# Optimization experiments

Measured on AMD Instinct MI355X. Metric: run time of the kernel, lower is better.

Reference implementation:

```python
import math
import jax, jax.numpy as jnp
import numpy as np

H = 16
D_MODEL = 1024
D_K = D_MODEL // H


def setup_inputs() -> dict:
    key = jax.random.key(0)
    ks = jax.random.split(key, 16)
    B, S = 2, 2048
    s = 1.0 / math.sqrt(D_MODEL)
    inp = {
        "q": jax.random.normal(ks[0], (B, S, D_MODEL), jnp.float32),
        "k": jax.random.normal(ks[1], (B, S, D_MODEL), jnp.float32),
        "v": jax.random.normal(ks[2], (B, S, D_MODEL), jnp.float32),
        "mask": jax.random.randint(ks[3], (B, S), 0, 2, jnp.int32),
        "Wq": jax.random.normal(ks[4], (D_MODEL, D_MODEL), jnp.float32) * s,
        "bq": jnp.zeros((D_MODEL,), jnp.float32),
        "Wk": jax.random.normal(ks[5], (D_MODEL, D_MODEL), jnp.float32) * s,
        "bk": jnp.zeros((D_MODEL,), jnp.float32),
        "Wv": jax.random.normal(ks[6], (D_MODEL, D_MODEL), jnp.float32) * s,
        "bv": jnp.zeros((D_MODEL,), jnp.float32),
        "Wp": jax.random.normal(ks[7], (D_MODEL, D_MODEL), jnp.float32) * s,
        "bp": jnp.zeros((D_MODEL,), jnp.float32),
        "gamma": jnp.ones((D_MODEL,), jnp.float32),
        "beta": jnp.zeros((D_MODEL,), jnp.float32),
    }
    return inp


def reference(q, k, v, mask, Wq, bq, Wk, bk, Wv, bv, Wp, bp, gamma, beta):
    B, S, _ = q.shape
    residual = q
    # projections -> [B, H, S, D_K]
    def split_heads(x):
        return x.reshape(B, S, H, D_K).transpose(0, 2, 1, 3)
    qh = split_heads(q @ Wq + bq)
    kh = split_heads(k @ Wk + bk)
    vh = split_heads(v @ Wv + bv)
    # scores [B, H, S, S]
    scores = jnp.einsum("bhqd,bhkd->bhqk", qh, kh) / math.sqrt(D_K)
    m = mask[:, None, None, :]  # [B,1,1,S_k]
    scores = jnp.where(m == 0, -1e9, scores)
    attn = jax.nn.softmax(scores, axis=-1)  # dropout is identity in eval
    out = jnp.einsum("bhqk,bhkd->bhqd", attn, vh)
    out = out.transpose(0, 2, 1, 3).reshape(B, S, D_MODEL)
    out = out @ Wp + bp
    x = residual + out
    # LayerNorm over last dim, eps=1e-5 (torch default)
    mu = jnp.mean(x, axis=-1, keepdims=True)
    var = jnp.mean((x - mu) ** 2, axis=-1, keepdims=True)
    out = (x - mu) * jax.lax.rsqrt(var + 1e-5) * gamma + beta
    return (out, attn)
```

## Files before the change

kernel.cpp:

```cpp
#include <hip/hip_runtime.h>
#include <hip/hip_bf16.h>

#define HN 16
#define DM 1024
#define DKH 64
#define BB 2
#define SS 2048
#define NT (BB*SS)
#define BK 32

using bf16   = __bf16;
using bf16x4 = __attribute__((ext_vector_type(4))) __bf16;
using bf16x8 = __attribute__((ext_vector_type(8))) __bf16;
using f32x4  = __attribute__((ext_vector_type(4))) float;

__device__ __forceinline__ void gload16(bf16* lds, const bf16* g) {
    __builtin_amdgcn_global_load_lds(
        (const __attribute__((address_space(1))) unsigned int*)g,
        (__attribute__((address_space(3))) unsigned int*)lds, 16, 0, 0);
}

__global__ __launch_bounds__(256) void convert_qkv(
    const float* __restrict__ q, const float* __restrict__ k,
    const float* __restrict__ v, bf16* __restrict__ dst)
{
    const int z = blockIdx.z;
    const float* src = (z == 0) ? q : (z == 1) ? k : v;
    bf16* d = dst + (size_t)z * NT * DM;
    int i = blockIdx.x * 256 + threadIdx.x;
    const int n4 = NT * DM / 4;
    if (i < n4) {
        float4 f = ((const float4*)src)[i];
        bf16x4 o = { (bf16)f.x, (bf16)f.y, (bf16)f.z, (bf16)f.w };
        ((bf16x4*)d)[i] = o;
    }
}

__global__ __launch_bounds__(256) void transpose_w(
    const float* __restrict__ Wq, const float* __restrict__ Wk,
    const float* __restrict__ Wv, const float* __restrict__ Wp,
    bf16* __restrict__ dst)
{
    const int z = blockIdx.z;
    const float* W = (z == 0) ? Wq : (z == 1) ? Wk : (z == 2) ? Wv : Wp;
    bf16* WT = dst + (size_t)z * DM * DM;
    __shared__ float t[64][65];
    const int tx = threadIdx.x;
    const int r0 = blockIdx.y * 64, c0 = blockIdx.x * 64;
    {
        const int row = tx >> 2, cb = (tx & 3) * 16;
        const float4* src = (const float4*)(W + (size_t)(r0 + row) * DM + c0 + cb);
        #pragma unroll
        for (int i = 0; i < 4; i++) {
            float4 f = src[i];
            t[row][cb + i*4 + 0] = f.x; t[row][cb + i*4 + 1] = f.y;
            t[row][cb + i*4 + 2] = f.z; t[row][cb + i*4 + 3] = f.w;
        }
    }
    __syncthreads();
    {
        const int n = tx >> 2, kb = (tx & 3) * 16;
        bf16 buf[16];
        #pragma unroll
        for (int i = 0; i < 16; i++) buf[i] = (bf16)t[kb + i][n];
        bf16* outp = WT + (size_t)(c0 + n) * DM + r0 + kb;
        *(bf16x8*)(outp)     = *(bf16x8*)(&buf[0]);
        *(bf16x8*)(outp + 8) = *(bf16x8*)(&buf[8]);
    }
}

__device__ __forceinline__ void gemm_core_128(
    const bf16* __restrict__ A, const bf16* __restrict__ Bt,
    int row0, int col0, bf16* As, bf16* Bs, f32x4 (&acc)[4][4])
{
    const int t = threadIdx.x;
    const int lane = t & 63, w = t >> 6;
    const int wr = w >> 1, wc = w & 1;
    const int lg = lane >> 4, l16 = lane & 15;
    const int srow = lane >> 2, scol = (lane & 3) * 8;
    const bf16* gA0 = A  + (size_t)(row0 + w*32 +      srow) * DM + scol;
    const bf16* gA1 = A  + (size_t)(row0 + w*32 + 16 + srow) * DM + scol;
    const bf16* gB0 = Bt + (size_t)(col0 + w*32 +      srow) * DM + scol;
    const bf16* gB1 = Bt + (size_t)(col0 + w*32 + 16 + srow) * DM + scol;
    bf16* lA0 = As + (w*32     ) * BK;
    bf16* lA1 = As + (w*32 + 16) * BK;
    bf16* lB0 = Bs + (w*32     ) * BK;
    bf16* lB1 = Bs + (w*32 + 16) * BK;

    for (int k0 = 0; k0 < DM; k0 += BK) {
        gload16(lA0, gA0 + k0);
        gload16(lA1, gA1 + k0);
        gload16(lB0, gB0 + k0);
        gload16(lB1, gB1 + k0);
        __syncthreads();
        bf16x8 af[4], bfr[4];
        #pragma unroll
        for (int m = 0; m < 4; m++)
            af[m] = *(const bf16x8*)(As + (wr*64 + m*16 + l16) * BK + lg*8);
        #pragma unroll
        for (int n = 0; n < 4; n++)
            bfr[n] = *(const bf16x8*)(Bs + (wc*64 + n*16 + l16) * BK + lg*8);
        #pragma unroll
        for (int m = 0; m < 4; m++)
            #pragma unroll
            for (int n = 0; n < 4; n++)
                acc[m][n] = __builtin_amdgcn_mfma_f32_16x16x32_bf16(af[m], bfr[n], acc[m][n], 0, 0, 0);
        __syncthreads();
    }
}

__global__ __launch_bounds__(256) void gemm_qkv(
    const bf16* __restrict__ qkvb, const bf16* __restrict__ wT,
    const float* __restrict__ bq, const float* __restrict__ bk,
    const float* __restrict__ bv, bf16* __restrict__ outbase)
{
    __shared__ __align__(16) bf16 As[128 * BK];
    __shared__ __align__(16) bf16 Bs[128 * BK];
    const int z = blockIdx.z;
    const bf16* A;
    const bf16* Bt;
    int row0, col0;
    if (z != 2) {
        A    = qkvb + (size_t)z * NT * DM;
        Bt   = wT   + (size_t)z * DM * DM;
        row0 = blockIdx.y * 128;
        col0 = blockIdx.x * 128;
    } else {
        A    = wT   + (size_t)2 * DM * DM;
        Bt   = qkvb + (size_t)2 * NT * DM;
        row0 = blockIdx.x * 128;
        col0 = blockIdx.y * 128;
    }

    f32x4 acc[4][4] = {};
    gemm_core_128(A, Bt, row0, col0, As, Bs, acc);

    const int t = threadIdx.x, lane = t & 63, w = t >> 6;
    const int wr = w >> 1, wc = w & 1, lg = lane >> 4, l16 = lane & 15;

    if (z == 0) {
        bf16* outp = outbase;
        const float qscale = 0.125f * 1.44269504f;
        #pragma unroll
        for (int m = 0; m < 4; m++) {
            #pragma unroll
            for (int n = 0; n < 4; n++) {
                const int col = col0 + wc*64 + n*16 + l16;
                const float bcol = bq[col];
                const int h = col >> 6, dk = col & 63;
                #pragma unroll
                for (int r = 0; r < 4; r++) {
                    const int row = row0 + wr*64 + m*16 + lg*4 + r;
                    const int b = row >> 11, s = row & (SS - 1);
                    const float val = (acc[m][n][r] + bcol) * qscale;
                    outp[(((size_t)b*HN + h)*SS + s)*DKH + dk] = (bf16)val;
                }
            }
        }
    } else if (z == 1) {
        bf16* outp = outbase + (size_t)NT * DM;
        #pragma unroll
        for (int m = 0; m < 4; m++) {
            #pragma unroll
            for (int n = 0; n < 4; n++) {
                const int col = col0 + wc*64 + n*16 + l16;
                const float bcol = bk[col];
                const int h = col >> 6, d = col & 63;
                #pragma unroll
                for (int r = 0; r < 4; r++) {
                    const int row = row0 + wr*64 + m*16 + lg*4 + r;
                    const int b = row >> 11, s = row & (SS - 1);
                    const float val = acc[m][n][r] + bcol;
                    const size_t bh = (size_t)b*HN + h;
                    const size_t idx = bh*SS*DKH
                        + (size_t)(((s>>4)*2 + (d>>5))*512)
                        + ((s&15)*4 + ((d>>3)&3))*8 + (d&7);
                    outp[idx] = (bf16)val;
                }
            }
        }
    } else {
        bf16* outp = outbase + (size_t)2 * NT * DM;
        #pragma unroll
        for (int m = 0; m < 4; m++) {
            #pragma unroll
            for (int n = 0; n < 4; n++) {
                const int tok = col0 + wc*64 + n*16 + l16;
                const int b = tok >> 11, s = tok & (SS - 1);
                #pragma unroll
                for (int r = 0; r < 4; r++) {
                    const int hdk = row0 + wr*64 + m*16 + lg*4 + r;
                    const int h = hdk >> 6, dk = hdk & 63;
                    const float val = acc[m][n][r] + bv[hdk];
                    const size_t bh = (size_t)b*HN + h;
                    const size_t idx = bh*SS*DKH
                        + (size_t)(((s>>5)*4 + (dk>>4))*512)
                        + ((dk&15)*4 + ((s>>3)&3))*8 + (s&7);
                    outp[idx] = (bf16)val;
                }
            }
        }
    }
}

__global__ __launch_bounds__(256) void attn_kernel(
    const bf16* __restrict__ Qh, const bf16* __restrict__ Kswz,
    const bf16* __restrict__ Vswz, const int* __restrict__ mask,
    float* __restrict__ attn, bf16* __restrict__ Ob)
{
    __shared__ float bias_s[SS];
    const int hwid = blockIdx.x;
    const int vid  = (hwid & 7) * 64 + (hwid >> 3);
    const int bh = vid >> 4;
    const int b  = bh >> 4;
    const int q0 = (vid & 15) * 128;
    const bf16* Kb = Kswz + (size_t)bh * SS * DKH;
    const bf16* Vb = Vswz + (size_t)bh * SS * DKH;
    const bf16* Q  = Qh   + (size_t)bh * SS * DKH;
    const int t = threadIdx.x, w = t >> 6, lane = t & 63;
    const int lg = lane >> 4, l16 = lane & 15;
    const int lp = (l16 << 2) | lg;

    for (int i = t; i < SS; i += 256)
        bias_s[i] = mask[b * SS + i] ? 0.0f : -1.44269504e9f;

    bf16x8 qf[2][2];
    #pragma unroll
    for (int tl = 0; tl < 2; tl++) {
        const bf16* qp = Q + (size_t)(q0 + w*32 + tl*16 + l16)*DKH + lg*8;
        qf[tl][0] = *(const bf16x8*)(qp);
        qf[tl][1] = *(const bf16x8*)(qp + 32);
    }
    __syncthreads();

    float l_[2] = {0.f, 0.f};
    bf16x8 kc0 = *(const bf16x8*)(Kb + lp*8);
    bf16x8 kc1 = *(const bf16x8*)(Kb + 512 + lp*8);
    for (int c = 0; c < 128; c++) {
        const int cn = (c + 1 < 128) ? c + 1 : 127;
        bf16x8 kn0 = *(const bf16x8*)(Kb + (size_t)(cn*2    )*512 + lp*8);
        bf16x8 kn1 = *(const bf16x8*)(Kb + (size_t)(cn*2 + 1)*512 + lp*8);
        const float4 b4 = *(const float4*)(&bias_s[c*16 + lg*4]);
        #pragma unroll
        for (int tl = 0; tl < 2; tl++) {
            f32x4 st = {0.f, 0.f, 0.f, 0.f};
            st = __builtin_amdgcn_mfma_f32_16x16x32_bf16(kc0, qf[tl][0], st, 0, 0, 0);
            st = __builtin_amdgcn_mfma_f32_16x16x32_bf16(kc1, qf[tl][1], st, 0, 0, 0);
            l_[tl] += exp2f(st[0] + b4.x) + exp2f(st[1] + b4.y)
                    + exp2f(st[2] + b4.z) + exp2f(st[3] + b4.w);
        }
        kc0 = kn0; kc1 = kn1;
    }
    float inv_l[2];
    #pragma unroll
    for (int tl = 0; tl < 2; tl++) {
        float l = l_[tl];
        l += __shfl_xor(l, 16);
        l += __shfl_xor(l, 32);
        inv_l[tl] = 1.0f / l;
    }

    float* attn_base = attn + ((size_t)bh * SS + q0 + w*32) * SS;
    f32x4 oacc[2][4] = {};
    const int srcA = ((((2*lg)    ) & 3)*16 + l16) << 2;
    const int srcB = ((((2*lg) + 1) & 3)*16 + l16) << 2;
    const bool selT = (lg >= 2);
    const int  kseg = lane & 7;
    const bool selS = (kseg >> 2) != 0;
    const int  srow8 = lane >> 3;
    const int srcS0 = ((kseg & 3)*16 +     srow8) << 2;
    const int srcS1 = ((kseg & 3)*16 + 8 + srow8) << 2;

    bf16x8 ck[4], cv[4];
    #pragma unroll
    for (int h = 0; h < 4; h++) ck[h] = *(const bf16x8*)(Kb + (size_t)h*512 + lp*8);
    #pragma unroll
    for (int n = 0; n < 4; n++) cv[n] = *(const bf16x8*)(Vb + (size_t)n*512 + lp*8);

    for (int j = 0; j < 64; j++) {
        bf16x8 nk[4], nv[4];
        const bool have = (j + 1) < 64;
        if (have) {
            #pragma unroll
            for (int h = 0; h < 4; h++)
                nk[h] = *(const bf16x8*)(Kb + (size_t)((j+1)*4 + h)*512 + lp*8);
            #pragma unroll
            for (int n = 0; n < 4; n++)
                nv[n] = *(const bf16x8*)(Vb + (size_t)((j+1)*4 + n)*512 + lp*8);
        }
        const float4 b40 = *(const float4*)(&bias_s[(2*j    )*16 + lg*4]);
        const float4 b41 = *(const float4*)(&bias_s[(2*j + 1)*16 + lg*4]);
        #pragma unroll
        for (int tl = 0; tl < 2; tl++) {
            f32x4 s0 = {0.f, 0.f, 0.f, 0.f};
            s0 = __builtin_amdgcn_mfma_f32_16x16x32_bf16(ck[0], qf[tl][0], s0, 0, 0, 0);
            s0 = __builtin_amdgcn_mfma_f32_16x16x32_bf16(ck[1], qf[tl][1], s0, 0, 0, 0);
            f32x4 s1 = {0.f, 0.f, 0.f, 0.f};
            s1 = __builtin_amdgcn_mfma_f32_16x16x32_bf16(ck[2], qf[tl][0], s1, 0, 0, 0);
            s1 = __builtin_amdgcn_mfma_f32_16x16x32_bf16(ck[3], qf[tl][1], s1, 0, 0, 0);
            const float p00 = exp2f(s0[0] + b40.x), p01 = exp2f(s0[1] + b40.y);
            const float p02 = exp2f(s0[2] + b40.z), p03 = exp2f(s0[3] + b40.w);
            const float p10 = exp2f(s1[0] + b41.x), p11 = exp2f(s1[1] + b41.y);
            const float p12 = exp2f(s1[2] + b41.z), p13 = exp2f(s1[3] + b41.w);
            bf16x4 pk0 = { (bf16)p00, (bf16)p01, (bf16)p02, (bf16)p03 };
            bf16x4 pk1 = { (bf16)p10, (bf16)p11, (bf16)p12, (bf16)p13 };
            int2 k0d = *(int2*)&pk0;
            int2 k1d = *(int2*)&pk1;
            int dd0t0 = __builtin_amdgcn_ds_bpermute(srcA, k0d.x);
            int dd0t1 = __builtin_amdgcn_ds_bpermute(srcA, k1d.x);
            int dd1t0 = __builtin_amdgcn_ds_bpermute(srcA, k0d.y);
            int dd1t1 = __builtin_amdgcn_ds_bpermute(srcA, k1d.y);
            int dd2t0 = __builtin_amdgcn_ds_bpermute(srcB, k0d.x);
            int dd2t1 = __builtin_amdgcn_ds_bpermute(srcB, k1d.x);
            int dd3t0 = __builtin_amdgcn_ds_bpermute(srcB, k0d.y);
            int dd3t1 = __builtin_amdgcn_ds_bpermute(srcB, k1d.y);
            union { int4 i; bf16x8 h; } pa;
            pa.i.x = selT ? dd0t1 : dd0t0;
            pa.i.y = selT ? dd1t1 : dd1t0;
            pa.i.z = selT ? dd2t1 : dd2t0;
            pa.i.w = selT ? dd3t1 : dd3t0;
            #pragma unroll
            for (int n = 0; n < 4; n++)
                oacc[tl][n] = __builtin_amdgcn_mfma_f32_16x16x32_bf16(pa.h, cv[n], oacc[tl][n], 0, 0, 0);
            const float il = inv_l[tl];
            f32x4 pv0 = { p00*il, p01*il, p02*il, p03*il };
            f32x4 pv1 = { p10*il, p11*il, p12*il, p13*il };
            #pragma unroll
            for (int i = 0; i < 2; i++) {
                const int srcS = i ? srcS1 : srcS0;
                f32x4 outv;
                #pragma unroll
                for (int d = 0; d < 4; d++) {
                    int v0 = __builtin_amdgcn_ds_bpermute(srcS, __float_as_int(pv0[d]));
                    int v1 = __builtin_amdgcn_ds_bpermute(srcS, __float_as_int(pv1[d]));
                    outv[d] = __int_as_float(selS ? v1 : v0);
                }
                *(f32x4*)(attn_base + (size_t)(tl*16 + i*8 + srow8)*SS + j*32 + kseg*4) = outv;
            }
        }
        #pragma unroll
        for (int h = 0; h < 4; h++) ck[h] = nk[h];
        #pragma unroll
        for (int n = 0; n < 4; n++) cv[n] = nv[n];
    }

    const int hh = bh & 15;
    #pragma unroll
    for (int tl = 0; tl < 2; tl++) {
        #pragma unroll
        for (int r = 0; r < 4; r++) {
            const float il = __shfl(inv_l[tl], lg*4 + r);
            const int srow = q0 + w*32 + tl*16 + lg*4 + r;
            #pragma unroll
            for (int n = 0; n < 4; n++) {
                const float val = oacc[tl][n][r] * il;
                Ob[((size_t)b*SS + srow)*DM + hh*DKH + n*16 + l16] = (bf16)val;
            }
        }
    }
}

__global__ __launch_bounds__(256) void gemm_out(
    const bf16* __restrict__ Ob, const bf16* __restrict__ WpT,
    const float* __restrict__ bp, const float* __restrict__ resid,
    float* __restrict__ out)
{
    __shared__ __align__(16) bf16 As[128 * BK];
    __shared__ __align__(16) bf16 Bs[128 * BK];
    const int row0 = blockIdx.y * 128, col0 = blockIdx.x * 128;
    f32x4 acc[4][4] = {};
    gemm_core_128(Ob, WpT, row0, col0, As, Bs, acc);

    const int t = threadIdx.x, lane = t & 63, w = t >> 6;
    const int wr = w >> 1, wc = w & 1, lg = lane >> 4, l16 = lane & 15;
    #pragma unroll
    for (int m = 0; m < 4; m++) {
        #pragma unroll
        for (int n = 0; n < 4; n++) {
            const int col = col0 + wc*64 + n*16 + l16;
            const float bcol = bp[col];
            #pragma unroll
            for (int r = 0; r < 4; r++) {
                const int row = row0 + wr*64 + m*16 + lg*4 + r;
                const size_t idx = (size_t)row * DM + col;
                out[idx] = acc[m][n][r] + bcol + resid[idx];
            }
        }
    }
}

__global__ __launch_bounds__(256) void ln_kernel(
    float* __restrict__ x, const float* __restrict__ gamma,
    const float* __restrict__ beta)
{
    const int row = blockIdx.x, t = threadIdx.x;
    float4 v = ((const float4*)(x + (size_t)row * DM))[t];
    float s  = v.x + v.y + v.z + v.w;
    float s2 = v.x*v.x + v.y*v.y + v.z*v.z + v.w*v.w;
    #pragma unroll
    for (int off = 32; off; off >>= 1) {
        s  += __shfl_xor(s, off);
        s2 += __shfl_xor(s2, off);
    }
    __shared__ float rs_[4], rs2_[4];
    const int w = t >> 6;
    if ((t & 63) == 0) { rs_[w] = s; rs2_[w] = s2; }
    __syncthreads();
    s  = rs_[0] + rs_[1] + rs_[2] + rs_[3];
    s2 = rs2_[0] + rs2_[1] + rs2_[2] + rs2_[3];
    const float mu   = s * (1.0f / DM);
    const float var  = s2 * (1.0f / DM) - mu * mu;
    const float rstd = rsqrtf(var + 1e-5f);
    float4 g  = ((const float4*)gamma)[t];
    float4 bb = ((const float4*)beta)[t];
    float4 o;
    o.x = (v.x - mu) * rstd * g.x + bb.x;
    o.y = (v.y - mu) * rstd * g.y + bb.y;
    o.z = (v.z - mu) * rstd * g.z + bb.z;
    o.w = (v.w - mu) * rstd * g.w + bb.w;
    ((float4*)(x + (size_t)row * DM))[t] = o;
}

extern "C" void kernel_launch(void* const* d_in, const int* in_sizes, int n_in,
                              void* d_out, int out_size, void* d_ws, size_t ws_size,
                              hipStream_t stream)
{
    const float* q     = (const float*)d_in[0];
    const float* k     = (const float*)d_in[1];
    const float* v     = (const float*)d_in[2];
    const int*   mask  = (const int*)  d_in[3];
    const float* Wq    = (const float*)d_in[4];
    const float* bq    = (const float*)d_in[5];
    const float* Wk    = (const float*)d_in[6];
    const float* bk    = (const float*)d_in[7];
    const float* Wv    = (const float*)d_in[8];
    const float* bv    = (const float*)d_in[9];
    const float* Wp    = (const float*)d_in[10];
    const float* bp    = (const float*)d_in[11];
    const float* gamma = (const float*)d_in[12];
    const float* beta  = (const float*)d_in[13];

    float* out  = (float*)d_out;
    float* attn = out + (size_t)NT * DM;

    char* wsb = (char*)d_ws;
    bf16* qb   = (bf16*)wsb;
    bf16* wT   = (bf16*)(wsb + 25165824);
    bf16* Qh   = (bf16*)(wsb + 33554432);
    bf16* Ob   = (bf16*)(wsb + 58720256);
    bf16* Kswz = Qh + (size_t)NT * DM;
    bf16* Vswz = Qh + (size_t)2 * NT * DM;

    convert_qkv<<<dim3(4096, 1, 3), 256, 0, stream>>>(q, k, v, qb);
    transpose_w<<<dim3(16, 16, 4), 256, 0, stream>>>(Wq, Wk, Wv, Wp, wT);
    gemm_qkv   <<<dim3(8, 32, 3),  256, 0, stream>>>(qb, wT, bq, bk, bv, Qh);
    attn_kernel<<<dim3(512, 1),    256, 0, stream>>>(Qh, Kswz, Vswz, mask, attn, Ob);
    gemm_out   <<<dim3(8, 32),     256, 0, stream>>>(Ob, wT + 3*1048576, bp, q, out);
    ln_kernel  <<<4096,            256, 0, stream>>>(out, gamma, beta);
}
```

Before: 325.0 us.

## Halve attention query tile per block to double grid size and occupancy

Each attention block now handles 64 query rows (16 per wave) instead of 128, so the grid grows from 512 to 1024 blocks and the per-wave two-tile loop collapses to a single tile. The launch bounds gain a min-blocks hint of 4 to cap register use and raise occupancy. The aim is to fill the 256 CUs more evenly and hide the memory latency of the large attn-matrix writes. In exchange, each K/V tile is reused by half as many queries, so K/V global reads roughly double and the mask-bias LDS setup is repeated per block.

Result: slower. 384.5 us (+18.3%).

```diff
diff --git a/kernel.cpp b/kernel.cpp
--- a/kernel.cpp
+++ b/kernel.cpp
@@ -203,17 +203,17 @@
     }
 }
 
-__global__ __launch_bounds__(256) void attn_kernel(
+__global__ __launch_bounds__(256, 4) void attn_kernel(
     const bf16* __restrict__ Qh, const bf16* __restrict__ Kswz,
     const bf16* __restrict__ Vswz, const int* __restrict__ mask,
     float* __restrict__ attn, bf16* __restrict__ Ob)
 {
     __shared__ float bias_s[SS];
     const int hwid = blockIdx.x;
-    const int vid  = (hwid & 7) * 64 + (hwid >> 3);
-    const int bh = vid >> 4;
+    const int vid  = (hwid & 7) * 128 + (hwid >> 3);
+    const int bh = vid >> 5;
     const int b  = bh >> 4;
-    const int q0 = (vid & 15) * 128;
+    const int q0 = (vid & 31) * 64;
     const bf16* Kb = Kswz + (size_t)bh * SS * DKH;
     const bf16* Vb = Vswz + (size_t)bh * SS * DKH;
     const bf16* Q  = Qh   + (size_t)bh * SS * DKH;
@@ -224,16 +224,15 @@
     for (int i = t; i < SS; i += 256)
         bias_s[i] = mask[b * SS + i] ? 0.0f : -1.44269504e9f;
 
-    bf16x8 qf[2][2];
-    #pragma unroll
-    for (int tl = 0; tl < 2; tl++) {
-        const bf16* qp = Q + (size_t)(q0 + w*32 + tl*16 + l16)*DKH + lg*8;
-        qf[tl][0] = *(const bf16x8*)(qp);
-        qf[tl][1] = *(const bf16x8*)(qp + 32);
+    bf16x8 qf[2];
+    {
+        const bf16* qp = Q + (size_t)(q0 + w*16 + l16)*DKH + lg*8;
+        qf[0] = *(const bf16x8*)(qp);
+        qf[1] = *(const bf16x8*)(qp + 32);
     }
     __syncthreads();
 
-    float l_[2] = {0.f, 0.f};
+    float l_ = 0.f;
     bf16x8 kc0 = *(const bf16x8*)(Kb + lp*8);
     bf16x8 kc1 = *(const bf16x8*)(Kb + 512 + lp*8);
     for (int c = 0; c < 128; c++) {
@@ -241,27 +240,23 @@
         bf16x8 kn0 = *(const bf16x8*)(Kb + (size_t)(cn*2    )*512 + lp*8);
         bf16x8 kn1 = *(const bf16x8*)(Kb + (size_t)(cn*2 + 1)*512 + lp*8);
         const float4 b4 = *(const float4*)(&bias_s[c*16 + lg*4]);
-        #pragma unroll
-        for (int tl = 0; tl < 2; tl++) {
-            f32x4 st = {0.f, 0.f, 0.f, 0.f};
-            st = __builtin_amdgcn_mfma_f32_16x16x32_bf16(kc0, qf[tl][0], st, 0, 0, 0);
-            st = __builtin_amdgcn_mfma_f32_16x16x32_bf16(kc1, qf[tl][1], st, 0, 0, 0);
-            l_[tl] += exp2f(st[0] + b4.x) + exp2f(st[1] + b4.y)
-                    + exp2f(st[2] + b4.z) + exp2f(st[3] + b4.w);
-        }
+        f32x4 st = {0.f, 0.f, 0.f, 0.f};
+        st = __builtin_amdgcn_mfma_f32_16x16x32_bf16(kc0, qf[0], st, 0, 0, 0);
+        st = __builtin_amdgcn_mfma_f32_16x16x32_bf16(kc1, qf[1], st, 0, 0, 0);
+        l_ += exp2f(st[0] + b4.x) + exp2f(st[1] + b4.y)
+            + exp2f(st[2] + b4.z) + exp2f(st[3] + b4.w);
         kc0 = kn0; kc1 = kn1;
     }
-    float inv_l[2];
-    #pragma unroll
-    for (int tl = 0; tl < 2; tl++) {
-        float l = l_[tl];
+    float inv_l;
+    {
+        float l = l_;
         l += __shfl_xor(l, 16);
         l += __shfl_xor(l, 32);
-        inv_l[tl] = 1.0f / l;
-    }
-
-    float* attn_base = attn + ((size_t)bh * SS + q0 + w*32) * SS;
-    f32x4 oacc[2][4] = {};
+        inv_l = 1.0f / l;
+    }
+
+    float* attn_base = attn + ((size_t)bh * SS + q0 + w*16) * SS;
+    f32x4 oacc[4] = {};
     const int srcA = ((((2*lg)    ) & 3)*16 + l16) << 2;
     const int srcB = ((((2*lg) + 1) & 3)*16 + l16) << 2;
     const bool selT = (lg >= 2);
@@ -290,14 +285,13 @@
         }
         const float4 b40 = *(const float4*)(&bias_s[(2*j    )*16 + lg*4]);
         const float4 b41 = *(const float4*)(&bias_s[(2*j + 1)*16 + lg*4]);
-        #pragma unroll
-        for (int tl = 0; tl < 2; tl++) {
+        {
             f32x4 s0 = {0.f, 0.f, 0.f, 0.f};
-            s0 = __builtin_amdgcn_mfma_f32_16x16x32_bf16(ck[0], qf[tl][0], s0, 0, 0, 0);
-            s0 = __builtin_amdgcn_mfma_f32_16x16x32_bf16(ck[1], qf[tl][1], s0, 0, 0, 0);
+            s0 = __builtin_amdgcn_mfma_f32_16x16x32_bf16(ck[0], qf[0], s0, 0, 0, 0);
+            s0 = __builtin_amdgcn_mfma_f32_16x16x32_bf16(ck[1], qf[1], s0, 0, 0, 0);
             f32x4 s1 = {0.f, 0.f, 0.f, 0.f};
-            s1 = __builtin_amdgcn_mfma_f32_16x16x32_bf16(ck[2], qf[tl][0], s1, 0, 0, 0);
-            s1 = __builtin_amdgcn_mfma_f32_16x16x32_bf16(ck[3], qf[tl][1], s1, 0, 0, 0);
+            s1 = __builtin_amdgcn_mfma_f32_16x16x32_bf16(ck[2], qf[0], s1, 0, 0, 0);
+            s1 = __builtin_amdgcn_mfma_f32_16x16x32_bf16(ck[3], qf[1], s1, 0, 0, 0);
             const float p00 = exp2f(s0[0] + b40.x), p01 = exp2f(s0[1] + b40.y);
             const float p02 = exp2f(s0[2] + b40.z), p03 = exp2f(s0[3] + b40.w);
             const float p10 = exp2f(s1[0] + b41.x), p11 = exp2f(s1[1] + b41.y);
@@ -321,8 +315,8 @@
             pa.i.w = selT ? dd3t1 : dd3t0;
             #pragma unroll
             for (int n = 0; n < 4; n++)
-                oacc[tl][n] = __builtin_amdgcn_mfma_f32_16x16x32_bf16(pa.h, cv[n], oacc[tl][n], 0, 0, 0);
-            const float il = inv_l[tl];
+                oacc[n] = __builtin_amdgcn_mfma_f32_16x16x32_bf16(pa.h, cv[n], oacc[n], 0, 0, 0);
+            const float il = inv_l;
             f32x4 pv0 = { p00*il, p01*il, p02*il, p03*il };
             f32x4 pv1 = { p10*il, p11*il, p12*il, p13*il };
             #pragma unroll
@@ -335,7 +329,7 @@
                     int v1 = __builtin_amdgcn_ds_bpermute(srcS, __float_as_int(pv1[d]));
                     outv[d] = __int_as_float(selS ? v1 : v0);
                 }
-                *(f32x4*)(attn_base + (size_t)(tl*16 + i*8 + srow8)*SS + j*32 + kseg*4) = outv;
+                *(f32x4*)(attn_base + (size_t)(i*8 + srow8)*SS + j*32 + kseg*4) = outv;
             }
         }
         #pragma unroll
@@ -346,16 +340,13 @@
 
     const int hh = bh & 15;
     #pragma unroll
-    for (int tl = 0; tl < 2; tl++) {
-        #pragma unroll
-        for (int r = 0; r < 4; r++) {
-            const float il = __shfl(inv_l[tl], lg*4 + r);
-            const int srow = q0 + w*32 + tl*16 + lg*4 + r;
-            #pragma unroll
-            for (int n = 0; n < 4; n++) {
-                const float val = oacc[tl][n][r] * il;
-                Ob[((size_t)b*SS + srow)*DM + hh*DKH + n*16 + l16] = (bf16)val;
-            }
+    for (int r = 0; r < 4; r++) {
+        const float il = __shfl(inv_l, lg*4 + r);
+        const int srow = q0 + w*16 + lg*4 + r;
+        #pragma unroll
+        for (int n = 0; n < 4; n++) {
+            const float val = oacc[n][r] * il;
+            Ob[((size_t)b*SS + srow)*DM + hh*DKH + n*16 + l16] = (bf16)val;
         }
     }
 }
@@ -454,7 +445,7 @@
     convert_qkv<<<dim3(4096, 1, 3), 256, 0, stream>>>(q, k, v, qb);
     transpose_w<<<dim3(16, 16, 4), 256, 0, stream>>>(Wq, Wk, Wv, Wp, wT);
     gemm_qkv   <<<dim3(8, 32, 3),  256, 0, stream>>>(qb, wT, bq, bk, bv, Qh);
-    attn_kernel<<<dim3(512, 1),    256, 0, stream>>>(Qh, Kswz, Vswz, mask, attn, Ob);
+    attn_kernel<<<dim3(1024, 1),   256, 0, stream>>>(Qh, Kswz, Vswz, mask, attn, Ob);
     gemm_out   <<<dim3(8, 32),     256, 0, stream>>>(Ob, wT + 3*1048576, bp, q, out);
     ln_kernel  <<<4096,            256, 0, stream>>>(out, gamma, beta);
 }
```

## Split attention key range across two wave groups with LDS reduction

Applied to the files above, without the earlier changes.

The attention kernel now runs 512 threads per block: two groups of four waves each take half of the key sequence for both the row-sum pass and the P·V/attn-write pass. Partial row sums and partial output accumulators are combined through shared memory, with a sync between stages. The register double-buffered K/V prefetch is replaced by direct loads each iteration. The aim is more waves in flight per block, to hide memory latency on the large attn store. The cost is extra LDS, sync overhead, and register pressure under launch_bounds(512,4).

New measurement: 348.9 us. 1.07x slower.

```diff
diff --git a/kernel.cpp b/kernel.cpp
--- a/kernel.cpp
+++ b/kernel.cpp
@@ -203,12 +203,14 @@
     }
 }
 
-__global__ __launch_bounds__(256) void attn_kernel(
+__global__ __launch_bounds__(512, 4) void attn_kernel(
     const bf16* __restrict__ Qh, const bf16* __restrict__ Kswz,
     const bf16* __restrict__ Vswz, const int* __restrict__ mask,
     float* __restrict__ attn, bf16* __restrict__ Ob)
 {
     __shared__ float bias_s[SS];
+    __shared__ float l_red[2][4][2][16];
+    __shared__ float ored[4][32][68];
     const int hwid = blockIdx.x;
     const int vid  = (hwid & 7) * 64 + (hwid >> 3);
     const int bh = vid >> 4;
@@ -218,26 +220,28 @@
     const bf16* Vb = Vswz + (size_t)bh * SS * DKH;
     const bf16* Q  = Qh   + (size_t)bh * SS * DKH;
     const int t = threadIdx.x, w = t >> 6, lane = t & 63;
+    const int qw = w & 3, kw = w >> 2;
     const int lg = lane >> 4, l16 = lane & 15;
     const int lp = (l16 << 2) | lg;
 
-    for (int i = t; i < SS; i += 256)
+    for (int i = t; i < SS; i += 512)
         bias_s[i] = mask[b * SS + i] ? 0.0f : -1.44269504e9f;
 
     bf16x8 qf[2][2];
     #pragma unroll
     for (int tl = 0; tl < 2; tl++) {
-        const bf16* qp = Q + (size_t)(q0 + w*32 + tl*16 + l16)*DKH + lg*8;
+        const bf16* qp = Q + (size_t)(q0 + qw*32 + tl*16 + l16)*DKH + lg*8;
         qf[tl][0] = *(const bf16x8*)(qp);
         qf[tl][1] = *(const bf16x8*)(qp + 32);
     }
     __syncthreads();
 
+    const int c0 = kw * 64, c1 = c0 + 64;
     float l_[2] = {0.f, 0.f};
-    bf16x8 kc0 = *(const bf16x8*)(Kb + lp*8);
-    bf16x8 kc1 = *(const bf16x8*)(Kb + 512 + lp*8);
-    for (int c = 0; c < 128; c++) {
-        const int cn = (c + 1 < 128) ? c + 1 : 127;
+    bf16x8 kc0 = *(const bf16x8*)(Kb + (size_t)(c0*2    )*512 + lp*8);
+    bf16x8 kc1 = *(const bf16x8*)(Kb + (size_t)(c0*2 + 1)*512 + lp*8);
+    for (int c = c0; c < c1; c++) {
+        const int cn = (c + 1 < c1) ? c + 1 : c1 - 1;
         bf16x8 kn0 = *(const bf16x8*)(Kb + (size_t)(cn*2    )*512 + lp*8);
         bf16x8 kn1 = *(const bf16x8*)(Kb + (size_t)(cn*2 + 1)*512 + lp*8);
         const float4 b4 = *(const float4*)(&bias_s[c*16 + lg*4]);
@@ -251,16 +255,22 @@
         }
         kc0 = kn0; kc1 = kn1;
     }
+    #pragma unroll
+    for (int tl = 0; tl < 2; tl++) {
+        l_[tl] += __shfl_xor(l_[tl], 16);
+        l_[tl] += __shfl_xor(l_[tl], 32);
+    }
+    if (lane < 16) {
+        l_red[kw][qw][0][l16] = l_[0];
+        l_red[kw][qw][1][l16] = l_[1];
+    }
+    __syncthreads();
     float inv_l[2];
     #pragma unroll
-    for (int tl = 0; tl < 2; tl++) {
-        float l = l_[tl];
-        l += __shfl_xor(l, 16);
-        l += __shfl_xor(l, 32);
-        inv_l[tl] = 1.0f / l;
-    }
-
-    float* attn_base = attn + ((size_t)bh * SS + q0 + w*32) * SS;
+    for (int tl = 0; tl < 2; tl++)
+        inv_l[tl] = 1.0f / (l_[tl] + l_red[kw ^ 1][qw][tl][l16]);
+
+    float* attn_base = attn + ((size_t)bh * SS + q0 + qw*32) * SS;
     f32x4 oacc[2][4] = {};
     const int srcA = ((((2*lg)    ) & 3)*16 + l16) << 2;
     const int srcB = ((((2*lg) + 1) & 3)*16 + l16) << 2;
@@ -271,23 +281,15 @@
     const int srcS0 = ((kseg & 3)*16 +     srow8) << 2;
     const int srcS1 = ((kseg & 3)*16 + 8 + srow8) << 2;
 
-    bf16x8 ck[4], cv[4];
-    #pragma unroll
-    for (int h = 0; h < 4; h++) ck[h] = *(const bf16x8*)(Kb + (size_t)h*512 + lp*8);
-    #pragma unroll
-    for (int n = 0; n < 4; n++) cv[n] = *(const bf16x8*)(Vb + (size_t)n*512 + lp*8);
-
-    for (int j = 0; j < 64; j++) {
-        bf16x8 nk[4], nv[4];
-        const bool have = (j + 1) < 64;
-        if (have) {
-            #pragma unroll
-            for (int h = 0; h < 4; h++)
-                nk[h] = *(const bf16x8*)(Kb + (size_t)((j+1)*4 + h)*512 + lp*8);
-            #pragma unroll
-            for (int n = 0; n < 4; n++)
-                nv[n] = *(const bf16x8*)(Vb + (size_t)((j+1)*4 + n)*512 + lp*8);
-        }
+    const int j0 = kw * 32, j1 = j0 + 32;
+    for (int j = j0; j < j1; j++) {
+        bf16x8 ck[4], cv[4];
+        #pragma unroll
+        for (int h = 0; h < 4; h++)
+            ck[h] = *(const bf16x8*)(Kb + (size_t)(j*4 + h)*512 + lp*8);
+        #pragma unroll
+        for (int n = 0; n < 4; n++)
+            cv[n] = *(const bf16x8*)(Vb + (size_t)(j*4 + n)*512 + lp*8);
         const float4 b40 = *(const float4*)(&bias_s[(2*j    )*16 + lg*4]);
         const float4 b41 = *(const float4*)(&bias_s[(2*j + 1)*16 + lg*4]);
         #pragma unroll
@@ -338,23 +340,32 @@
                 *(f32x4*)(attn_base + (size_t)(tl*16 + i*8 + srow8)*SS + j*32 + kseg*4) = outv;
             }
         }
-        #pragma unroll
-        for (int h = 0; h < 4; h++) ck[h] = nk[h];
-        #pragma unroll
-        for (int n = 0; n < 4; n++) cv[n] = nv[n];
-    }
-
-    const int hh = bh & 15;
-    #pragma unroll
-    for (int tl = 0; tl < 2; tl++) {
-        #pragma unroll
-        for (int r = 0; r < 4; r++) {
-            const float il = __shfl(inv_l[tl], lg*4 + r);
-            const int srow = q0 + w*32 + tl*16 + lg*4 + r;
-            #pragma unroll
-            for (int n = 0; n < 4; n++) {
-                const float val = oacc[tl][n][r] * il;
-                Ob[((size_t)b*SS + srow)*DM + hh*DKH + n*16 + l16] = (bf16)val;
+    }
+
+    if (kw == 0) {
+        #pragma unroll
+        for (int tl = 0; tl < 2; tl++)
+            #pragma unroll
+            for (int n = 0; n < 4; n++)
+                #pragma unroll
+                for (int r = 0; r < 4; r++)
+                    ored[qw][tl*16 + lg*4 + r][n*16 + l16] = oacc[tl][n][r];
+    }
+    __syncthreads();
+    if (kw == 1) {
+        const int hh = bh & 15;
+        #pragma unroll
+        for (int tl = 0; tl < 2; tl++) {
+            #pragma unroll
+            for (int r = 0; r < 4; r++) {
+                const float il = __shfl(inv_l[tl], lg*4 + r);
+                const int srow = q0 + qw*32 + tl*16 + lg*4 + r;
+                #pragma unroll
+                for (int n = 0; n < 4; n++) {
+                    const float val = (oacc[tl][n][r]
+                        + ored[qw][tl*16 + lg*4 + r][n*16 + l16]) * il;
+                    Ob[((size_t)b*SS + srow)*DM + hh*DKH + n*16 + l16] = (bf16)val;
+                }
             }
         }
     }
@@ -454,7 +465,7 @@
     convert_qkv<<<dim3(4096, 1, 3), 256, 0, stream>>>(q, k, v, qb);
     transpose_w<<<dim3(16, 16, 4), 256, 0, stream>>>(Wq, Wk, Wv, Wp, wT);
     gemm_qkv   <<<dim3(8, 32, 3),  256, 0, stream>>>(qb, wT, bq, bk, bv, Qh);
-    attn_kernel<<<dim3(512, 1),    256, 0, stream>>>(Qh, Kswz, Vswz, mask, attn, Ob);
+    attn_kernel<<<dim3(512, 1),    512, 0, stream>>>(Qh, Kswz, Vswz, mask, attn, Ob);
     gemm_out   <<<dim3(8, 32),     256, 0, stream>>>(Ob, wT + 3*1048576, bp, q, out);
     ln_kernel  <<<4096,            256, 0, stream>>>(out, gamma, beta);
 }
```
